# Kernel tuning notes

Hardware: AMD Instinct MI355X
Metric: run time of the kernel (lower is better)

## Reference

```python
import jax, jax.numpy as jnp
import numpy as np

MARGIN = 1.0


def setup_inputs() -> dict:
    key = jax.random.key(0)
    k1, k2, k3 = jax.random.split(key, 3)
    n, d = 8192, 128
    feat1 = jax.random.normal(k1, (n, d), dtype=jnp.float32)
    feat2 = jax.random.normal(k2, (n, d), dtype=jnp.float32)
    # similarity labels in {+1, -1}, as expected by HingeEmbeddingLoss
    simi = (2 * jax.random.randint(k3, (n, n), 0, 2) - 1).astype(jnp.int32)
    return {"feat1": feat1, "feat2": feat2, "simi": simi}


def reference(feat1, feat2, simi):
    # logits[i,j] = -||feat1_i - feat2_j||^2, computed without the O(n*m*d) expand
    sq1 = jnp.sum(feat1 * feat1, axis=-1, keepdims=True)          # [n, 1]
    sq2 = jnp.sum(feat2 * feat2, axis=-1)                          # [m]
    cross = jnp.einsum('nd,md->nm', feat1, feat2)                  # [n, m]
    logits = -(sq1 + sq2[None, :] - 2.0 * cross)                   # [n, m]
    probs = jax.nn.softmax(logits, axis=1)                         # [n, m]
    # HingeEmbeddingLoss: x if y==1 else max(0, margin - x); mean reduction
    loss = jnp.where(simi == 1, probs, jnp.maximum(0.0, MARGIN - probs))
    return jnp.mean(loss)
```

## Files before the change

kernel.cpp:

```cpp
#include <hip/hip_runtime.h>
#include <hip/hip_bf16.h>
#include <stdint.h>

#define N 8192
#define D 128
#define NCHUNK 16
#define CHUNK (N / NCHUNK)
#define RT 128
#define CT 64
#define NTILES (CHUNK / CT)
#define NBLK (N / RT * NCHUNK)

typedef short bf16x8 __attribute__((ext_vector_type(8)));
typedef float f32x4 __attribute__((ext_vector_type(4)));
typedef unsigned int uint32;

#define OFF_ACC   0u
#define OFF_SQ2   1024u
#define OFF_BCNT  (OFF_SQ2 + N * 4u)
#define OFF_M     (OFF_BCNT + NBLK * 4u)
#define OFF_L     (OFF_M + NCHUNK * N * 4u)
#define OFF_S     (OFF_L + NCHUNK * N * 4u)
#define OFF_F1    (OFF_S + NCHUNK * N * 4u)
#define OFF_F2    (OFF_F1 + N * D * 2u)

__global__ __launch_bounds__(256)
void prep_kernel(const float* __restrict__ f1, const float* __restrict__ f2,
                 unsigned short* __restrict__ f1b, unsigned short* __restrict__ f2b,
                 float* __restrict__ sq2) {
    const int w    = blockIdx.x * 4 + (threadIdx.x >> 6);
    const int lane = threadIdx.x & 63;
    for (int row = w; row < N; row += 1024) {
        float a0 = f1[row * D + lane];
        float a1 = f1[row * D + 64 + lane];
        float b0 = f2[row * D + lane];
        float b1 = f2[row * D + 64 + lane];
        __hip_bfloat16 t;
        t = __float2bfloat16(a0); f1b[row * D + lane]      = *(unsigned short*)&t;
        t = __float2bfloat16(a1); f1b[row * D + 64 + lane] = *(unsigned short*)&t;
        t = __float2bfloat16(b0); f2b[row * D + lane]      = *(unsigned short*)&t;
        t = __float2bfloat16(b1); f2b[row * D + 64 + lane] = *(unsigned short*)&t;
        float ss = b0 * b0 + b1 * b1;
        #pragma unroll
        for (int off = 32; off > 0; off >>= 1) ss += __shfl_xor(ss, off);
        if (lane == 0) sq2[row] = ss;
    }
}

__global__ __launch_bounds__(256)
void main_kernel(const unsigned short* __restrict__ f1b,
                 const unsigned short* __restrict__ f2b,
                 const float* __restrict__ sq2,
                 const int* __restrict__ simi,
                 float* __restrict__ pm, float* __restrict__ pl, float* __restrict__ ps,
                 uint32* __restrict__ blockcnt) {
    __shared__ unsigned short ldsB[CT * D];
    __shared__ uint32 cred[4];

    const int tid  = threadIdx.x;
    const int wave = tid >> 6;
    const int lane = tid & 63;
    const int lo   = lane & 15;
    const int hi   = lane >> 4;

    const int rowtile = blockIdx.x;
    const int chunk   = blockIdx.y;
    const int rbase   = rowtile * RT + wave * 32;
    const int cbase0  = chunk * CHUNK;

    bf16x8 afrag[2][4];
    #pragma unroll
    for (int a = 0; a < 2; a++) {
        const unsigned short* ap = f1b + (size_t)(rbase + a * 16 + lo) * D + hi * 8;
        #pragma unroll
        for (int kk = 0; kk < 4; kk++)
            afrag[a][kk] = *reinterpret_cast<const bf16x8*>(ap + kk * 32);
    }

    const int sq_ = (tid >> 4);
    const int sg_ = tid & 15;

    const int* simi_p = simi + (size_t)(rbase + hi * 4) * N + cbase0 + 4 * lo;

    float m[2][4], l[2][4], s[2][4];
    #pragma unroll
    for (int a = 0; a < 2; a++)
        #pragma unroll
        for (int r = 0; r < 4; r++) { m[a][r] = -1e30f; l[a][r] = 0.f; s[a][r] = 0.f; }
    uint32 cnt = 0;

    for (int t = 0; t < NTILES; t++) {
        const int cbase = cbase0 + t * CT;

        int4 mkv[2][4];
        #pragma unroll
        for (int a = 0; a < 2; a++)
            #pragma unroll
            for (int r = 0; r < 4; r++)
                mkv[a][r] = *reinterpret_cast<const int4*>(simi_p + (size_t)(a * 16 + r) * N);

        __syncthreads();
        #pragma unroll
        for (int it = 0; it < 4; it++) {
            int q = it * 16 + sq_;
            int c = 4 * (q & 15) + (q >> 4);
            const uint4 v = *reinterpret_cast<const uint4*>(f2b + (size_t)(cbase + c) * D + sg_ * 8);
            *reinterpret_cast<uint4*>(ldsB + q * D + ((sg_ ^ (q & 15)) * 8)) = v;
        }
        __syncthreads();

        uint32 mb[2][4];
        #pragma unroll
        for (int a = 0; a < 2; a++)
            #pragma unroll
            for (int r = 0; r < 4; r++) {
                int4 v = mkv[a][r];
                uint32 nib = (uint32)(v.x == 1) | ((uint32)(v.y == 1) << 1) |
                             ((uint32)(v.z == 1) << 2) | ((uint32)(v.w == 1) << 3);
                mb[a][r] = nib;
                cnt += 4u - __popc(nib);
            }

        f32x4 acc[2][4];
        #pragma unroll
        for (int cf = 0; cf < 4; cf++) {
            acc[0][cf] = (f32x4){0.f, 0.f, 0.f, 0.f};
            acc[1][cf] = (f32x4){0.f, 0.f, 0.f, 0.f};
            const int brow = cf * 16 + lo;
            #pragma unroll
            for (int kk = 0; kk < 4; kk++) {
                int g = kk * 4 + hi;
                bf16x8 b = *reinterpret_cast<const bf16x8*>(
                    ldsB + brow * D + ((g ^ (brow & 15)) * 8));
                acc[0][cf] = __builtin_amdgcn_mfma_f32_16x16x32_bf16(afrag[0][kk], b, acc[0][cf], 0, 0, 0);
                acc[1][cf] = __builtin_amdgcn_mfma_f32_16x16x32_bf16(afrag[1][kk], b, acc[1][cf], 0, 0, 0);
            }
        }

        f32x4 sqv = *reinterpret_cast<const f32x4*>(sq2 + cbase0 + t * CT + 4 * lo);
        #pragma unroll
        for (int a = 0; a < 2; a++)
            #pragma unroll
            for (int r = 0; r < 4; r++) {
                float lg[4];
                #pragma unroll
                for (int cf = 0; cf < 4; cf++)
                    lg[cf] = 2.0f * acc[a][cf][r] - sqv[cf];
                float tm = fmaxf(fmaxf(lg[0], lg[1]), fmaxf(lg[2], lg[3]));
                float mn = fmaxf(m[a][r], tm);
                float al = __expf(m[a][r] - mn);
                m[a][r] = mn;
                float p[4];
                #pragma unroll
                for (int cf = 0; cf < 4; cf++) p[cf] = __expf(lg[cf] - mn);
                l[a][r] = l[a][r] * al + ((p[0] + p[1]) + (p[2] + p[3]));
                float sm = 0.f;
                #pragma unroll
                for (int cf = 0; cf < 4; cf++)
                    sm += ((mb[a][r] >> cf) & 1u) ? p[cf] : 0.f;
                s[a][r] = s[a][r] * al + sm;
            }
        simi_p += CT;
    }

    #pragma unroll
    for (int a = 0; a < 2; a++)
        #pragma unroll
        for (int r = 0; r < 4; r++) {
            float M = m[a][r];
            #pragma unroll
            for (int off = 1; off < 16; off <<= 1)
                M = fmaxf(M, __shfl_xor(M, off));
            float sc = __expf(m[a][r] - M);
            float L = l[a][r] * sc, S = s[a][r] * sc;
            #pragma unroll
            for (int off = 1; off < 16; off <<= 1) {
                L += __shfl_xor(L, off);
                S += __shfl_xor(S, off);
            }
            if (lo == 0) {
                int row = rbase + a * 16 + hi * 4 + r;
                int idx = chunk * N + row;
                pm[idx] = M; pl[idx] = L; ps[idx] = S;
            }
        }

    #pragma unroll
    for (int off = 1; off < 64; off <<= 1) cnt += __shfl_xor(cnt, off);
    if (lane == 0) cred[wave] = cnt;
    __syncthreads();
    if (tid == 0)
        blockcnt[blockIdx.y * 64 + blockIdx.x] = cred[0] + cred[1] + cred[2] + cred[3];
}

__global__ void merge_kernel(const float* __restrict__ pm, const float* __restrict__ pl,
                             const float* __restrict__ ps, const uint32* __restrict__ blockcnt,
                             float* __restrict__ s_acc, uint32* __restrict__ neg_acc) {
    const int row = blockIdx.x * 256 + threadIdx.x;
    float M = -1e30f;
    #pragma unroll
    for (int k = 0; k < NCHUNK; k++) M = fmaxf(M, pm[k * N + row]);
    float L = 0.f, S = 0.f;
    #pragma unroll
    for (int k = 0; k < NCHUNK; k++) {
        float e = __expf(pm[k * N + row] - M);
        L += pl[k * N + row] * e;
        S += ps[k * N + row] * e;
    }
    float r = S / L;
    uint32 pc = (threadIdx.x < 32) ? blockcnt[blockIdx.x * 32 + threadIdx.x] : 0u;
    #pragma unroll
    for (int off = 32; off > 0; off >>= 1) {
        r  += __shfl_xor(r, off);
        pc += __shfl_xor(pc, off);
    }
    __shared__ float red[4];
    __shared__ uint32 redp[4];
    int lane = threadIdx.x & 63, w = threadIdx.x >> 6;
    if (lane == 0) { red[w] = r; redp[w] = pc; }
    __syncthreads();
    if (threadIdx.x == 0) {
        atomicAdd(s_acc, red[0] + red[1] + red[2] + red[3]);
        atomicAdd(neg_acc, redp[0] + redp[1] + redp[2] + redp[3]);
    }
}

__global__ void final_kernel(const float* __restrict__ s_acc, const uint32* __restrict__ neg_acc,
                             float* __restrict__ out) {
    double S = (double)s_acc[0];
    double C = (double)neg_acc[0];
    double n = (double)N;
    out[0] = (float)((2.0 * S + C - n) / (n * n));
}

extern "C" void kernel_launch(void* const* d_in, const int* in_sizes, int n_in,
                              void* d_out, int out_size, void* d_ws, size_t ws_size,
                              hipStream_t stream) {
    const float* f1   = (const float*)d_in[0];
    const float* f2   = (const float*)d_in[1];
    const int*   simi = (const int*)d_in[2];
    float* out = (float*)d_out;
    char* ws = (char*)d_ws;

    float*  acc_s    = (float*)(ws + OFF_ACC);
    uint32* acc_n    = (uint32*)(ws + OFF_ACC + 4);
    float*  sq2      = (float*)(ws + OFF_SQ2);
    uint32* blockcnt = (uint32*)(ws + OFF_BCNT);
    float*  pm       = (float*)(ws + OFF_M);
    float*  pl       = (float*)(ws + OFF_L);
    float*  ps       = (float*)(ws + OFF_S);
    unsigned short* f1b = (unsigned short*)(ws + OFF_F1);
    unsigned short* f2b = (unsigned short*)(ws + OFF_F2);

    hipMemsetAsync(ws + OFF_ACC, 0, 64, stream);
    prep_kernel<<<256, 256, 0, stream>>>(f1, f2, f1b, f2b, sq2);
    main_kernel<<<dim3(N / RT, NCHUNK), 256, 0, stream>>>(f1b, f2b, sq2, simi,
                                                          pm, pl, ps, blockcnt);
    merge_kernel<<<N / 256, 256, 0, stream>>>(pm, pl, ps, blockcnt, acc_s, acc_n);
    final_kernel<<<1, 1, 0, stream>>>(acc_s, acc_n, out);
}
```

Before: 407.0 us.

## Load B fragments directly from global, drop LDS staging and barriers

Removes the shared-memory staging of feat2 tiles and both __syncthreads per tile, so each wave reads its MFMA B operands straight from global memory (relying on L1/L2 for reuse across the four waves). The simi mask loads become nontemporal to avoid polluting cache, and mask decoding is moved after the MFMAs to overlap load latency. The trade-off is redundant global and cache traffic for B across waves and uncoalesced per-lane row access in exchange for no barriers or LDS.

```diff
diff --git a/kernel.cpp b/kernel.cpp
--- a/kernel.cpp
+++ b/kernel.cpp
@@ -13,6 +13,7 @@
 
 typedef short bf16x8 __attribute__((ext_vector_type(8)));
 typedef float f32x4 __attribute__((ext_vector_type(4)));
+typedef int   i32x4 __attribute__((ext_vector_type(4)));
 typedef unsigned int uint32;
 
 #define OFF_ACC   0u
@@ -54,7 +55,6 @@
                  const int* __restrict__ simi,
                  float* __restrict__ pm, float* __restrict__ pl, float* __restrict__ ps,
                  uint32* __restrict__ blockcnt) {
-    __shared__ unsigned short ldsB[CT * D];
     __shared__ uint32 cred[4];
 
     const int tid  = threadIdx.x;
@@ -77,10 +77,8 @@
             afrag[a][kk] = *reinterpret_cast<const bf16x8*>(ap + kk * 32);
     }
 
-    const int sq_ = (tid >> 4);
-    const int sg_ = tid & 15;
-
     const int* simi_p = simi + (size_t)(rbase + hi * 4) * N + cbase0 + 4 * lo;
+    const unsigned short* bp = f2b + (size_t)(cbase0 + 4 * lo) * D + hi * 8;
 
     float m[2][4], l[2][4], s[2][4];
     #pragma unroll
@@ -90,52 +88,38 @@
     uint32 cnt = 0;
 
     for (int t = 0; t < NTILES; t++) {
-        const int cbase = cbase0 + t * CT;
-
-        int4 mkv[2][4];
+        i32x4 mkv[2][4];
         #pragma unroll
         for (int a = 0; a < 2; a++)
             #pragma unroll
             for (int r = 0; r < 4; r++)
-                mkv[a][r] = *reinterpret_cast<const int4*>(simi_p + (size_t)(a * 16 + r) * N);
-
-        __syncthreads();
-        #pragma unroll
-        for (int it = 0; it < 4; it++) {
-            int q = it * 16 + sq_;
-            int c = 4 * (q & 15) + (q >> 4);
-            const uint4 v = *reinterpret_cast<const uint4*>(f2b + (size_t)(cbase + c) * D + sg_ * 8);
-            *reinterpret_cast<uint4*>(ldsB + q * D + ((sg_ ^ (q & 15)) * 8)) = v;
-        }
-        __syncthreads();
-
-        uint32 mb[2][4];
-        #pragma unroll
-        for (int a = 0; a < 2; a++)
-            #pragma unroll
-            for (int r = 0; r < 4; r++) {
-                int4 v = mkv[a][r];
-                uint32 nib = (uint32)(v.x == 1) | ((uint32)(v.y == 1) << 1) |
-                             ((uint32)(v.z == 1) << 2) | ((uint32)(v.w == 1) << 3);
-                mb[a][r] = nib;
-                cnt += 4u - __popc(nib);
-            }
+                mkv[a][r] = __builtin_nontemporal_load(
+                    reinterpret_cast<const i32x4*>(simi_p + (size_t)(a * 16 + r) * N));
 
         f32x4 acc[2][4];
         #pragma unroll
         for (int cf = 0; cf < 4; cf++) {
             acc[0][cf] = (f32x4){0.f, 0.f, 0.f, 0.f};
             acc[1][cf] = (f32x4){0.f, 0.f, 0.f, 0.f};
-            const int brow = cf * 16 + lo;
             #pragma unroll
             for (int kk = 0; kk < 4; kk++) {
-                int g = kk * 4 + hi;
-                bf16x8 b = *reinterpret_cast<const bf16x8*>(
-                    ldsB + brow * D + ((g ^ (brow & 15)) * 8));
+                bf16x8 b = *reinterpret_cast<const bf16x8*>(bp + (size_t)cf * D + kk * 32);
                 acc[0][cf] = __builtin_amdgcn_mfma_f32_16x16x32_bf16(afrag[0][kk], b, acc[0][cf], 0, 0, 0);
                 acc[1][cf] = __builtin_amdgcn_mfma_f32_16x16x32_bf16(afrag[1][kk], b, acc[1][cf], 0, 0, 0);
             }
         }
+
+        uint32 mb[2][4];
+        #pragma unroll
+        for (int a = 0; a < 2; a++)
+            #pragma unroll
+            for (int r = 0; r < 4; r++) {
+                i32x4 v = mkv[a][r];
+                uint32 nib = (uint32)(v[0] == 1) | ((uint32)(v[1] == 1) << 1) |
+                             ((uint32)(v[2] == 1) << 2) | ((uint32)(v[3] == 1) << 3);
+                mb[a][r] = nib;
+                cnt += 4u - __popc(nib);
+            }
 
         f32x4 sqv = *reinterpret_cast<const f32x4*>(sq2 + cbase0 + t * CT + 4 * lo);
         #pragma unroll
@@ -161,6 +145,7 @@
                 s[a][r] = s[a][r] * al + sm;
             }
         simi_p += CT;
+        bp += (size_t)CT * D;
     }
 
     #pragma unroll
```

Result: slower. 446.6 us (+9.7%).
